# Kernel tuning notes

Measured on AMD Instinct MI355X. Metric: run time of the kernel, lower is better.

Reference implementation:

```python
import jax, jax.numpy as jnp
import numpy as np

B, H, N, C = 4, 16, 1024, 64
D = H * C  # d_model = 1024


def setup_inputs() -> dict:
    key = jax.random.key(0)
    ks = jax.random.split(key, 6)
    q = jax.random.normal(ks[0], (B, H, N, C), dtype=jnp.float32)
    k = jax.random.normal(ks[1], (B, H, N, C), dtype=jnp.float32)
    v = jax.random.normal(ks[2], (B, H, N, C), dtype=jnp.float32)
    pe = jax.random.normal(ks[3], (1, H, N, N), dtype=jnp.float32)
    # Mlp(h*c): fc1 D->D, SiLU, fc2 D->D (stored as [in, out] for x @ W)
    w1 = jax.random.normal(ks[4], (D, D), dtype=jnp.float32) * (D ** -0.5)
    b1 = jnp.zeros((D,), dtype=jnp.float32)
    w2 = jax.random.normal(ks[5], (D, D), dtype=jnp.float32) * (D ** -0.5)
    b2 = jnp.zeros((D,), dtype=jnp.float32)
    return {"q": q, "k": k, "v": v, "pe": pe,
            "w1": w1, "b1": b1, "w2": w2, "b2": b2}


def reference(q, k, v, pe, w1, b1, w2, b2):
    b, h, n, c = q.shape
    scale = c ** (-0.5)
    # scores: [b,h,n,n]; softmax FIRST, then add pe bias (post-softmax bias)
    scores = jnp.einsum('bhnc,bhmc->bhnm', q, k) * scale
    attn = pe + jax.nn.softmax(scores, axis=-1)
    ctx = jnp.einsum('bhnm,bhmc->bhnc', attn, v)
    # [b,h,n,c] -> [b,n,h*c]
    out = ctx.transpose(0, 2, 1, 3).reshape(b, n, h * c)
    # Mlp: fc1 -> SiLU -> fc2 (dropout is identity at eval)
    hdn = jax.nn.silu(out @ w1 + b1)
    return hdn @ w2 + b2
```

## Files before the change

### kernel.cpp

```cpp
#include <hip/hip_runtime.h>

#define B_ 4
#define H_ 16
#define N_ 1024
#define C_ 64
#define D_ 1024

typedef _Float16 half8 __attribute__((ext_vector_type(8)));
typedef _Float16 half4v __attribute__((ext_vector_type(4)));
typedef float f32x4 __attribute__((ext_vector_type(4)));
typedef float f32x16 __attribute__((ext_vector_type(16)));
typedef unsigned int uint4v __attribute__((ext_vector_type(4)));

#define MFMA16(a, b, c) __builtin_amdgcn_mfma_f32_16x16x32_f16(a, b, c, 0, 0, 0)
#define MFMA32(a, b, c) __builtin_amdgcn_mfma_f32_32x32x16_f16(a, b, c, 0, 0, 0)
#define SM_SHIFT 6.0f

static __device__ __forceinline__ unsigned pk2(float a, float b) {
  auto h = __builtin_amdgcn_cvt_pkrtz(a, b);
  return __builtin_bit_cast(unsigned, h);
}
static __device__ __forceinline__ void swap32(unsigned& a, unsigned& b) {
  asm volatile("v_permlane32_swap_b32 %0, %1" : "+v"(a), "+v"(b));
}
static __device__ __forceinline__ void gload16(const void* g, void* l) {
  __builtin_amdgcn_global_load_lds(
      (const __attribute__((address_space(1))) unsigned int*)g,
      (__attribute__((address_space(3))) unsigned int*)l, 16, 0, 0);
}

__global__ __launch_bounds__(256) void transpose_cvt(
    const float* __restrict__ in, _Float16* __restrict__ outp,
    int in_stride, int out_stride, long in_bstride, long out_bstride)
{
  __shared__ float t[64][65];
  const int tid = threadIdx.x;
  const int r0 = blockIdx.x * 64, c0 = blockIdx.y * 64;
  const float* inb = in + (size_t)blockIdx.z * in_bstride;
  _Float16* outb = outp + (size_t)blockIdx.z * out_bstride;
#pragma unroll
  for (int i = 0; i < 4; ++i) {
    int idx = i * 256 + tid;
    int r = idx >> 4, c4 = (idx & 15) << 2;
    float4 a = *(const float4*)(inb + (size_t)(r0 + r) * in_stride + c0 + c4);
    t[r][c4] = a.x; t[r][c4 + 1] = a.y; t[r][c4 + 2] = a.z; t[r][c4 + 3] = a.w;
  }
  __syncthreads();
#pragma unroll
  for (int i = 0; i < 2; ++i) {
    int idx = i * 256 + tid;
    int rr = idx >> 3, c8 = (idx & 7) << 3;
    half8 hv;
#pragma unroll
    for (int j = 0; j < 8; ++j) hv[j] = (_Float16)t[c8 + j][rr];
    *(half8*)(outb + (size_t)(c0 + rr) * out_stride + r0 + c8) = hv;
  }
}

__global__ __launch_bounds__(256, 1) void pev_kernel(
    const float* __restrict__ pe, const _Float16* __restrict__ vth,
    _Float16* __restrict__ xpe)
{
  __shared__ __align__(16) _Float16 a_lds[2][64][72];
  __shared__ __align__(16) _Float16 b_lds[2][256][72];
  const int tid = threadIdx.x;
  const int n0 = blockIdx.x * 64;
  const int h = blockIdx.y;
  const float* peb = pe + (size_t)h * N_ * N_ + (size_t)n0 * N_;

  const int lane = tid & 63, w = tid >> 6;
  const int l15 = lane & 15, quad = lane >> 4;
  const int wrow = (w >> 1) * 32, wcol = (w & 1) * 128;

  const int ar[4] = { tid >> 4, (256 + tid) >> 4, (512 + tid) >> 4, (768 + tid) >> 4 };
  const int ac4 = (tid & 15) << 2;
  const _Float16* bsrc[8];
  int brow[8], bk8[8];
#pragma unroll
  for (int i = 0; i < 8; ++i) {
    int idx = i * 256 + tid;
    int col = idx >> 3, k8 = (idx & 7) << 3;
    int b = col >> 6, c = col & 63;
    bsrc[i] = vth + ((size_t)(b * H_ + h) * C_ + c) * N_ + k8;
    brow[i] = col;
    bk8[i] = k8;
  }

  f32x4 acc[2][8];
#pragma unroll
  for (int rt = 0; rt < 2; ++rt)
#pragma unroll
    for (int ct = 0; ct < 8; ++ct) acc[rt][ct] = (f32x4){0.f, 0.f, 0.f, 0.f};

  float4 areg[4];
  half8 breg[8];
#pragma unroll
  for (int i = 0; i < 4; ++i) areg[i] = *(const float4*)(peb + (size_t)ar[i] * N_ + ac4);
#pragma unroll
  for (int i = 0; i < 8; ++i) breg[i] = *(const half8*)(bsrc[i]);
#pragma unroll
  for (int i = 0; i < 4; ++i) {
    half4v hv = {(_Float16)areg[i].x, (_Float16)areg[i].y,
                 (_Float16)areg[i].z, (_Float16)areg[i].w};
    *(half4v*)&a_lds[0][ar[i]][ac4] = hv;
  }
#pragma unroll
  for (int i = 0; i < 8; ++i) *(half8*)&b_lds[0][brow[i]][bk8[i]] = breg[i];
#pragma unroll
  for (int i = 0; i < 4; ++i)
    areg[i] = *(const float4*)(peb + (size_t)ar[i] * N_ + 64 + ac4);
#pragma unroll
  for (int i = 0; i < 8; ++i) breg[i] = *(const half8*)(bsrc[i] + 64);
  __syncthreads();

  for (int kt = 0; kt < 16; ++kt) {
    const int cur = kt & 1;
    if (kt < 15) {
#pragma unroll
      for (int i = 0; i < 4; ++i) {
        half4v hv = {(_Float16)areg[i].x, (_Float16)areg[i].y,
                     (_Float16)areg[i].z, (_Float16)areg[i].w};
        *(half4v*)&a_lds[cur ^ 1][ar[i]][ac4] = hv;
      }
#pragma unroll
      for (int i = 0; i < 8; ++i) *(half8*)&b_lds[cur ^ 1][brow[i]][bk8[i]] = breg[i];
    }
    if (kt < 14) {
      int m0 = (kt + 2) * 64;
#pragma unroll
      for (int i = 0; i < 4; ++i)
        areg[i] = *(const float4*)(peb + (size_t)ar[i] * N_ + m0 + ac4);
#pragma unroll
      for (int i = 0; i < 8; ++i) breg[i] = *(const half8*)(bsrc[i] + m0);
    }
#pragma unroll
    for (int s = 0; s < 2; ++s) {
      half8 af[2], bf[8];
#pragma unroll
      for (int rt = 0; rt < 2; ++rt)
        af[rt] = *(const half8*)&a_lds[cur][wrow + rt * 16 + l15][s * 32 + quad * 8];
#pragma unroll
      for (int ct = 0; ct < 8; ++ct)
        bf[ct] = *(const half8*)&b_lds[cur][wcol + ct * 16 + l15][s * 32 + quad * 8];
#pragma unroll
      for (int rt = 0; rt < 2; ++rt)
#pragma unroll
        for (int ct = 0; ct < 8; ++ct)
          acc[rt][ct] = MFMA16(af[rt], bf[ct], acc[rt][ct]);
    }
    __syncthreads();
  }

#pragma unroll
  for (int rt = 0; rt < 2; ++rt)
#pragma unroll
    for (int ct = 0; ct < 8; ++ct) {
      int col = wcol + ct * 16 + l15;
      int b = col >> 6, c = col & 63;
#pragma unroll
      for (int r = 0; r < 4; ++r) {
        int nrow = n0 + wrow + rt * 16 + quad * 4 + r;
        xpe[(size_t)(b * N_ + nrow) * D_ + h * C_ + c] = (_Float16)acc[rt][ct][r];
      }
    }
}

__global__ __launch_bounds__(256, 2) void attn_kernel(
    const float* __restrict__ q, const float* __restrict__ k,
    const _Float16* __restrict__ vth, const _Float16* __restrict__ xpe,
    _Float16* __restrict__ Xh)
{
  __shared__ __align__(16) _Float16 ks[2][2][64][72];
  __shared__ __align__(16) _Float16 vst[2][2][64][72];
  __shared__ float lbuf[128];

  const int tid = threadIdx.x;
  const int bh = blockIdx.x & 63;
  const int qt = blockIdx.x >> 6;
  const int h = bh & (H_ - 1);
  const int b = bh >> 4;
  const int q0 = qt * 128;

  const float* kb = k + (size_t)bh * N_ * C_;
  const _Float16* vb = vth + (size_t)bh * C_ * N_;

  const int lane = tid & 63;
  const int w = tid >> 6;
  const int l31 = lane & 31;
  const int hh = lane >> 5;

  const int sr = tid >> 4, sc4 = (tid & 15) << 2;
  const int vr = tid >> 3, vc8 = (tid & 7) << 3;

  half8 qf[4];
  const float* qrow = q + ((size_t)bh * N_ + q0 + 32 * w + l31) * C_;
#pragma unroll
  for (int sc = 0; sc < 4; ++sc) {
    const float* qp = qrow + 16 * sc + 8 * hh;
    float4 t0 = *(const float4*)qp;
    float4 t1 = *(const float4*)(qp + 4);
    half8 hv = { (_Float16)(t0.x * 0.125f), (_Float16)(t0.y * 0.125f),
                 (_Float16)(t0.z * 0.125f), (_Float16)(t0.w * 0.125f),
                 (_Float16)(t1.x * 0.125f), (_Float16)(t1.y * 0.125f),
                 (_Float16)(t1.z * 0.125f), (_Float16)(t1.w * 0.125f) };
    qf[sc] = hv;
  }

  f32x16 Os2[2];
  Os2[0] = (f32x16)(0.f); Os2[1] = (f32x16)(0.f);
  float l4[4] = {0.f, 0.f, 0.f, 0.f};

  float4 kreg[8];
  uint4 vreg[4];

#pragma unroll
  for (int s = 0; s < 2; ++s) {
#pragma unroll
    for (int i = 0; i < 4; ++i)
      kreg[s * 4 + i] = *(const float4*)(kb + (size_t)(s * 64 + sr + i * 16) * C_ + sc4);
#pragma unroll
    for (int i = 0; i < 2; ++i)
      vreg[s * 2 + i] = *(const uint4*)(vb + (size_t)(vr + i * 32) * N_ + s * 64 + vc8);
  }
#pragma unroll
  for (int s = 0; s < 2; ++s) {
#pragma unroll
    for (int i = 0; i < 4; ++i) {
      float4 kv = kreg[s * 4 + i];
      half4v hk = {(_Float16)kv.x, (_Float16)kv.y, (_Float16)kv.z, (_Float16)kv.w};
      *(half4v*)&ks[0][s][sr + i * 16][sc4] = hk;
    }
#pragma unroll
    for (int i = 0; i < 2; ++i) *(uint4*)&vst[0][s][vr + i * 32][vc8] = vreg[s * 2 + i];
  }
#pragma unroll
  for (int s = 0; s < 2; ++s) {
#pragma unroll
    for (int i = 0; i < 4; ++i)
      kreg[s * 4 + i] = *(const float4*)(kb + (size_t)(128 + s * 64 + sr + i * 16) * C_ + sc4);
#pragma unroll
    for (int i = 0; i < 2; ++i)
      vreg[s * 2 + i] = *(const uint4*)(vb + (size_t)(vr + i * 32) * N_ + 128 + s * 64 + vc8);
  }
  __syncthreads();

  for (int p = 0; p < 8; ++p) {
    const int cur = p & 1;
    if (p < 7) {
#pragma unroll
      for (int s = 0; s < 2; ++s) {
#pragma unroll
        for (int i = 0; i < 4; ++i) {
          float4 kv = kreg[s * 4 + i];
          half4v hk = {(_Float16)kv.x, (_Float16)kv.y, (_Float16)kv.z, (_Float16)kv.w};
          *(half4v*)&ks[cur ^ 1][s][sr + i * 16][sc4] = hk;
        }
#pragma unroll
        for (int i = 0; i < 2; ++i)
          *(uint4*)&vst[cur ^ 1][s][vr + i * 32][vc8] = vreg[s * 2 + i];
      }
    }
    if (p < 6) {
      int m0 = (p + 2) * 128;
#pragma unroll
      for (int s = 0; s < 2; ++s) {
#pragma unroll
        for (int i = 0; i < 4; ++i)
          kreg[s * 4 + i] = *(const float4*)(kb + (size_t)(m0 + s * 64 + sr + i * 16) * C_ + sc4);
#pragma unroll
        for (int i = 0; i < 2; ++i)
          vreg[s * 2 + i] = *(const uint4*)(vb + (size_t)(vr + i * 32) * N_ + m0 + s * 64 + vc8);
      }
    }

    half8 pa[2][4];
#pragma unroll
    for (int s = 0; s < 2; ++s) {
      f32x16 sacc2[2];
      sacc2[0] = (f32x16)(0.f); sacc2[1] = (f32x16)(0.f);
#pragma unroll
      for (int sc = 0; sc < 4; ++sc) {
        half8 ak0 = *(const half8*)&ks[cur][s][l31][16 * sc + 8 * hh];
        half8 ak1 = *(const half8*)&ks[cur][s][32 + l31][16 * sc + 8 * hh];
        sacc2[0] = MFMA32(ak0, qf[sc], sacc2[0]);
        sacc2[1] = MFMA32(ak1, qf[sc], sacc2[1]);
      }
#pragma unroll
      for (int kbt = 0; kbt < 2; ++kbt) {
        float pv[16];
#pragma unroll
        for (int r = 0; r < 16; ++r) {
          pv[r] = __expf(sacc2[kbt][r] - SM_SHIFT);
          l4[r & 3] += pv[r];
        }
#pragma unroll
        for (int sp = 0; sp < 2; ++sp) {
          const int rb = 8 * sp;
          unsigned wa = pk2(pv[rb + 0], pv[rb + 1]);
          unsigned wb = pk2(pv[rb + 4], pv[rb + 5]);
          unsigned wc = pk2(pv[rb + 2], pv[rb + 3]);
          unsigned wd = pk2(pv[rb + 6], pv[rb + 7]);
          swap32(wa, wb);
          swap32(wc, wd);
          uint4v pw = {wa, wc, wb, wd};
          pa[s][kbt * 2 + sp] = __builtin_bit_cast(half8, pw);
        }
      }
    }

#pragma unroll
    for (int s = 0; s < 2; ++s)
#pragma unroll
      for (int st = 0; st < 4; ++st) {
        half8 bv0 = *(const half8*)&vst[cur][s][l31][16 * st + 8 * hh];
        half8 bv1 = *(const half8*)&vst[cur][s][32 + l31][16 * st + 8 * hh];
        Os2[0] = MFMA32(pa[s][st], bv0, Os2[0]);
        Os2[1] = MFMA32(pa[s][st], bv1, Os2[1]);
      }

    __syncthreads();
  }

  float l = (l4[0] + l4[1]) + (l4[2] + l4[3]);
  l += __shfl_xor(l, 32);
  lbuf[32 * w + l31] = 1.0f / l;

#pragma unroll
  for (int reg = 0; reg < 16; ++reg) {
    const int qi = (reg & 3) + 8 * (reg >> 2) + 4 * hh;
    const float li = lbuf[32 * w + qi];
    const size_t row = (size_t)(b * N_ + q0 + 32 * w + qi);
#pragma unroll
    for (int ct = 0; ct < 2; ++ct) {
      size_t o = row * D_ + h * C_ + 32 * ct + l31;
      Xh[o] = (_Float16)(Os2[ct][reg] * li + (float)xpe[o]);
    }
  }
}

template <bool SILU, typename OT>
__global__ __launch_bounds__(256, 2) void mlp_kernel(
    const _Float16* __restrict__ X, const _Float16* __restrict__ Wt,
    const float* __restrict__ bias, OT* __restrict__ Y)
{
  __shared__ __align__(16) _Float16 a_lds[2][128 * 64];
  __shared__ __align__(16) _Float16 b_lds[2][64 * 64];
  const int tid = threadIdx.x;
  const int id = blockIdx.x;
  const int xcd = id & 7, j = id >> 3;
  const int m0 = (xcd * 4 + (j & 3)) * 128;
  const int n0 = (j >> 2) * 64;
  const int lane = tid & 63, w = tid >> 6;
  const int wr = (w >> 1) * 64, wc = (w & 1) * 32;
  const int l15 = lane & 15, quad = lane >> 4;

  const int lrow8 = lane >> 3;
  const int lg = lane & 7;

  f32x4 acc[4][2];
#pragma unroll
  for (int rt = 0; rt < 4; ++rt)
#pragma unroll
    for (int ct = 0; ct < 2; ++ct) acc[rt][ct] = (f32x4){0.f, 0.f, 0.f, 0.f};

#define STAGE_MLP(buf, k0)                                                     \
  {                                                                            \
    _Float16* abase = &a_lds[buf][(w * 4) * 8 * 64];                           \
    _Float16* bbase = &b_lds[buf][(w * 2) * 8 * 64];                           \
    _Float16* ab = abase;                                                      \
    _Float16* bb = bbase;                                                      \
    _Float16* dummy = ab; (void)dummy;                                         \
    int ar0 = w * 32;                                                          \
    int br0 = w * 16;                                                          \
    for (int jj = 0; jj < 4; ++jj) {                                           \
      int r = ar0 + jj * 8 + lrow8;                                            \
      const _Float16* src = X + (size_t)(m0 + r) * D_ + (k0) + ((lg ^ (r & 7)) << 3); \
      gload16(src, &a_lds[buf][(ar0 + jj * 8) * 64]);                          \
    }                                                                          \
    for (int jj = 0; jj < 2; ++jj) {                                           \
      int r = br0 + jj * 8 + lrow8;                                            \
      const _Float16* src = Wt + (size_t)(n0 + r) * D_ + (k0) + ((lg ^ (r & 7)) << 3); \
      gload16(src, &b_lds[buf][(br0 + jj * 8) * 64]);                          \
    }                                                                          \
  }

  STAGE_MLP(0, 0);
  __syncthreads();

  for (int kt = 0; kt < 16; ++kt) {
    const int cur = kt & 1;
    if (kt < 15) STAGE_MLP(cur ^ 1, (kt + 1) * 64);
#pragma unroll
    for (int s = 0; s < 2; ++s) {
      half8 af[4], bf[2];
#pragma unroll
      for (int rt = 0; rt < 4; ++rt) {
        int row = wr + rt * 16 + l15;
        af[rt] = *(const half8*)&a_lds[cur][row * 64 + (((s * 4 + quad) ^ (row & 7)) << 3)];
      }
#pragma unroll
      for (int ct = 0; ct < 2; ++ct) {
        int row = wc + ct * 16 + l15;
        bf[ct] = *(const half8*)&b_lds[cur][row * 64 + (((s * 4 + quad) ^ (row & 7)) << 3)];
      }
#pragma unroll
      for (int rt = 0; rt < 4; ++rt)
#pragma unroll
        for (int ct = 0; ct < 2; ++ct)
          acc[rt][ct] = MFMA16(af[rt], bf[ct], acc[rt][ct]);
    }
    __syncthreads();
  }
#undef STAGE_MLP

  float bv[2];
#pragma unroll
  for (int ct = 0; ct < 2; ++ct) bv[ct] = bias[n0 + wc + ct * 16 + l15];
#pragma unroll
  for (int rt = 0; rt < 4; ++rt)
#pragma unroll
    for (int ct = 0; ct < 2; ++ct)
#pragma unroll
      for (int r = 0; r < 4; ++r) {
        float val = acc[rt][ct][r] + bv[ct];
        if (SILU) val = val / (1.f + __expf(-val));
        int row = m0 + wr + rt * 16 + quad * 4 + r;
        int col = n0 + wc + ct * 16 + l15;
        Y[(size_t)row * D_ + col] = (OT)val;
      }
}

extern "C" void kernel_launch(void* const* d_in, const int* in_sizes, int n_in,
                              void* d_out, int out_size, void* d_ws, size_t ws_size,
                              hipStream_t stream) {
  const float* q  = (const float*)d_in[0];
  const float* k  = (const float*)d_in[1];
  const float* v  = (const float*)d_in[2];
  const float* pe = (const float*)d_in[3];
  const float* w1 = (const float*)d_in[4];
  const float* b1 = (const float*)d_in[5];
  const float* w2 = (const float*)d_in[6];
  const float* b2 = (const float*)d_in[7];
  float* out = (float*)d_out;

  _Float16* Xh  = (_Float16*)d_out;
  _Float16* vth = (_Float16*)((char*)d_out + (size_t)8 * 1024 * 1024);
  _Float16* xpeH1 = (_Float16*)d_ws;
  _Float16* w1t = (_Float16*)((char*)d_ws + (size_t)8 * 1024 * 1024);
  _Float16* w2t = (_Float16*)((char*)d_ws + (size_t)10 * 1024 * 1024);

  transpose_cvt<<<dim3(16, 16, 1), 256, 0, stream>>>(w1, w1t, D_, D_, 0, 0);
  transpose_cvt<<<dim3(16, 16, 1), 256, 0, stream>>>(w2, w2t, D_, D_, 0, 0);
  transpose_cvt<<<dim3(16, 1, B_ * H_), 256, 0, stream>>>(
      v, vth, C_, N_, (long)N_ * C_, (long)N_ * C_);
  pev_kernel<<<dim3(N_ / 64, H_), 256, 0, stream>>>(pe, vth, xpeH1);
  attn_kernel<<<dim3(B_ * H_ * (N_ / 128)), 256, 0, stream>>>(q, k, vth, xpeH1, Xh);
  mlp_kernel<true, _Float16><<<dim3(512), 256, 0, stream>>>(Xh, w1t, b1, xpeH1);
  mlp_kernel<false, float><<<dim3(512), 256, 0, stream>>>(xpeH1, w2t, b2, out);
}
```

Baseline: 245.2 us.

## Widen pe@V kernel to 512 threads and load V fragments directly from global in attention

The pe@V kernel now runs 8 waves per block instead of 4, halving per-thread staging loads and accumulator tiles so more waves are available to hide the fp32 pe stream. In the attention kernel, the V tile is no longer staged through LDS; each lane loads its MFMA B-fragments straight from the transposed fp16 V in global memory at the start of each iteration. This cuts LDS traffic and shared memory use, which may allow higher occupancy. The trade-off is that the V loads are no longer prefetched two iterations ahead, so their global latency sits right before the MFMAs, and loads are duplicated across waves. Dead pointer code in the MLP staging macro is also removed.

Measured after the change: 253.9 us. 1.04x slower.

```diff
diff --git a/kernel.cpp b/kernel.cpp
--- a/kernel.cpp
+++ b/kernel.cpp
@@ -57,7 +57,7 @@
   }
 }
 
-__global__ __launch_bounds__(256, 1) void pev_kernel(
+__global__ __launch_bounds__(512, 1) void pev_kernel(
     const float* __restrict__ pe, const _Float16* __restrict__ vth,
     _Float16* __restrict__ xpe)
 {
@@ -70,15 +70,15 @@
 
   const int lane = tid & 63, w = tid >> 6;
   const int l15 = lane & 15, quad = lane >> 4;
-  const int wrow = (w >> 1) * 32, wcol = (w & 1) * 128;
-
-  const int ar[4] = { tid >> 4, (256 + tid) >> 4, (512 + tid) >> 4, (768 + tid) >> 4 };
+  const int wrow = (w >> 2) * 32, wcol = (w & 3) * 64;
+
+  const int ar[2] = { tid >> 4, (512 + tid) >> 4 };
   const int ac4 = (tid & 15) << 2;
-  const _Float16* bsrc[8];
-  int brow[8], bk8[8];
-#pragma unroll
-  for (int i = 0; i < 8; ++i) {
-    int idx = i * 256 + tid;
+  const _Float16* bsrc[4];
+  int brow[4], bk8[4];
+#pragma unroll
+  for (int i = 0; i < 4; ++i) {
+    int idx = i * 512 + tid;
     int col = idx >> 3, k8 = (idx & 7) << 3;
     int b = col >> 6, c = col & 63;
     bsrc[i] = vth + ((size_t)(b * H_ + h) * C_ + c) * N_ + k8;
@@ -86,66 +86,66 @@
     bk8[i] = k8;
   }
 
-  f32x4 acc[2][8];
+  f32x4 acc[2][4];
 #pragma unroll
   for (int rt = 0; rt < 2; ++rt)
 #pragma unroll
-    for (int ct = 0; ct < 8; ++ct) acc[rt][ct] = (f32x4){0.f, 0.f, 0.f, 0.f};
-
-  float4 areg[4];
-  half8 breg[8];
-#pragma unroll
-  for (int i = 0; i < 4; ++i) areg[i] = *(const float4*)(peb + (size_t)ar[i] * N_ + ac4);
-#pragma unroll
-  for (int i = 0; i < 8; ++i) breg[i] = *(const half8*)(bsrc[i]);
-#pragma unroll
-  for (int i = 0; i < 4; ++i) {
+    for (int ct = 0; ct < 4; ++ct) acc[rt][ct] = (f32x4){0.f, 0.f, 0.f, 0.f};
+
+  float4 areg[2];
+  half8 breg[4];
+#pragma unroll
+  for (int i = 0; i < 2; ++i) areg[i] = *(const float4*)(peb + (size_t)ar[i] * N_ + ac4);
+#pragma unroll
+  for (int i = 0; i < 4; ++i) breg[i] = *(const half8*)(bsrc[i]);
+#pragma unroll
+  for (int i = 0; i < 2; ++i) {
     half4v hv = {(_Float16)areg[i].x, (_Float16)areg[i].y,
                  (_Float16)areg[i].z, (_Float16)areg[i].w};
     *(half4v*)&a_lds[0][ar[i]][ac4] = hv;
   }
 #pragma unroll
-  for (int i = 0; i < 8; ++i) *(half8*)&b_lds[0][brow[i]][bk8[i]] = breg[i];
-#pragma unroll
-  for (int i = 0; i < 4; ++i)
+  for (int i = 0; i < 4; ++i) *(half8*)&b_lds[0][brow[i]][bk8[i]] = breg[i];
+#pragma unroll
+  for (int i = 0; i < 2; ++i)
     areg[i] = *(const float4*)(peb + (size_t)ar[i] * N_ + 64 + ac4);
 #pragma unroll
-  for (int i = 0; i < 8; ++i) breg[i] = *(const half8*)(bsrc[i] + 64);
+  for (int i = 0; i < 4; ++i) breg[i] = *(const half8*)(bsrc[i] + 64);
   __syncthreads();
 
   for (int kt = 0; kt < 16; ++kt) {
     const int cur = kt & 1;
     if (kt < 15) {
 #pragma unroll
-      for (int i = 0; i < 4; ++i) {
+      for (int i = 0; i < 2; ++i) {
         half4v hv = {(_Float16)areg[i].x, (_Float16)areg[i].y,
                      (_Float16)areg[i].z, (_Float16)areg[i].w};
         *(half4v*)&a_lds[cur ^ 1][ar[i]][ac4] = hv;
       }
 #pragma unroll
-      for (int i = 0; i < 8; ++i) *(half8*)&b_lds[cur ^ 1][brow[i]][bk8[i]] = breg[i];
+      for (int i = 0; i < 4; ++i) *(half8*)&b_lds[cur ^ 1][brow[i]][bk8[i]] = breg[i];
     }
     if (kt < 14) {
       int m0 = (kt + 2) * 64;
 #pragma unroll
-      for (int i = 0; i < 4; ++i)
+      for (int i = 0; i < 2; ++i)
         areg[i] = *(const float4*)(peb + (size_t)ar[i] * N_ + m0 + ac4);
 #pragma unroll
-      for (int i = 0; i < 8; ++i) breg[i] = *(const half8*)(bsrc[i] + m0);
+      for (int i = 0; i < 4; ++i) breg[i] = *(const half8*)(bsrc[i] + m0);
     }
 #pragma unroll
     for (int s = 0; s < 2; ++s) {
-      half8 af[2], bf[8];
+      half8 af[2], bf[4];
 #pragma unroll
       for (int rt = 0; rt < 2; ++rt)
         af[rt] = *(const half8*)&a_lds[cur][wrow + rt * 16 + l15][s * 32 + quad * 8];
 #pragma unroll
-      for (int ct = 0; ct < 8; ++ct)
+      for (int ct = 0; ct < 4; ++ct)
         bf[ct] = *(const half8*)&b_lds[cur][wcol + ct * 16 + l15][s * 32 + quad * 8];
 #pragma unroll
       for (int rt = 0; rt < 2; ++rt)
 #pragma unroll
-        for (int ct = 0; ct < 8; ++ct)
+        for (int ct = 0; ct < 4; ++ct)
           acc[rt][ct] = MFMA16(af[rt], bf[ct], acc[rt][ct]);
     }
     __syncthreads();
@@ -154,7 +154,7 @@
 #pragma unroll
   for (int rt = 0; rt < 2; ++rt)
 #pragma unroll
-    for (int ct = 0; ct < 8; ++ct) {
+    for (int ct = 0; ct < 4; ++ct) {
       int col = wcol + ct * 16 + l15;
       int b = col >> 6, c = col & 63;
 #pragma unroll
@@ -171,7 +171,6 @@
     _Float16* __restrict__ Xh)
 {
   __shared__ __align__(16) _Float16 ks[2][2][64][72];
-  __shared__ __align__(16) _Float16 vst[2][2][64][72];
   __shared__ float lbuf[128];
 
   const int tid = threadIdx.x;
@@ -190,7 +189,9 @@
   const int hh = lane >> 5;
 
   const int sr = tid >> 4, sc4 = (tid & 15) << 2;
-  const int vr = tid >> 3, vc8 = (tid & 7) << 3;
+
+  const _Float16* vr0 = vb + (size_t)l31 * N_ + 8 * hh;
+  const _Float16* vr1 = vb + (size_t)(32 + l31) * N_ + 8 * hh;
 
   half8 qf[4];
   const float* qrow = q + ((size_t)bh * N_ + q0 + 32 * w + l31) * C_;
@@ -211,19 +212,14 @@
   float l4[4] = {0.f, 0.f, 0.f, 0.f};
 
   float4 kreg[8];
-  uint4 vreg[4];
-
-#pragma unroll
-  for (int s = 0; s < 2; ++s) {
+
+#pragma unroll
+  for (int s = 0; s < 2; ++s)
 #pragma unroll
     for (int i = 0; i < 4; ++i)
       kreg[s * 4 + i] = *(const float4*)(kb + (size_t)(s * 64 + sr + i * 16) * C_ + sc4);
 #pragma unroll
-    for (int i = 0; i < 2; ++i)
-      vreg[s * 2 + i] = *(const uint4*)(vb + (size_t)(vr + i * 32) * N_ + s * 64 + vc8);
-  }
-#pragma unroll
-  for (int s = 0; s < 2; ++s) {
+  for (int s = 0; s < 2; ++s)
 #pragma unroll
     for (int i = 0; i < 4; ++i) {
       float4 kv = kreg[s * 4 + i];
@@ -231,46 +227,42 @@
       *(half4v*)&ks[0][s][sr + i * 16][sc4] = hk;
     }
 #pragma unroll
-    for (int i = 0; i < 2; ++i) *(uint4*)&vst[0][s][vr + i * 32][vc8] = vreg[s * 2 + i];
-  }
-#pragma unroll
-  for (int s = 0; s < 2; ++s) {
+  for (int s = 0; s < 2; ++s)
 #pragma unroll
     for (int i = 0; i < 4; ++i)
       kreg[s * 4 + i] = *(const float4*)(kb + (size_t)(128 + s * 64 + sr + i * 16) * C_ + sc4);
-#pragma unroll
-    for (int i = 0; i < 2; ++i)
-      vreg[s * 2 + i] = *(const uint4*)(vb + (size_t)(vr + i * 32) * N_ + 128 + s * 64 + vc8);
-  }
   __syncthreads();
 
   for (int p = 0; p < 8; ++p) {
     const int cur = p & 1;
+
+    uint4 vfr[2][4][2];
+#pragma unroll
+    for (int s = 0; s < 2; ++s)
+#pragma unroll
+      for (int st = 0; st < 4; ++st) {
+        const int off = p * 128 + s * 64 + st * 16;
+        vfr[s][st][0] = *(const uint4*)(vr0 + off);
+        vfr[s][st][1] = *(const uint4*)(vr1 + off);
+      }
+
     if (p < 7) {
 #pragma unroll
-      for (int s = 0; s < 2; ++s) {
+      for (int s = 0; s < 2; ++s)
 #pragma unroll
         for (int i = 0; i < 4; ++i) {
           float4 kv = kreg[s * 4 + i];
           half4v hk = {(_Float16)kv.x, (_Float16)kv.y, (_Float16)kv.z, (_Float16)kv.w};
           *(half4v*)&ks[cur ^ 1][s][sr + i * 16][sc4] = hk;
         }
-#pragma unroll
-        for (int i = 0; i < 2; ++i)
-          *(uint4*)&vst[cur ^ 1][s][vr + i * 32][vc8] = vreg[s * 2 + i];
-      }
     }
     if (p < 6) {
       int m0 = (p + 2) * 128;
 #pragma unroll
-      for (int s = 0; s < 2; ++s) {
+      for (int s = 0; s < 2; ++s)
 #pragma unroll
         for (int i = 0; i < 4; ++i)
           kreg[s * 4 + i] = *(const float4*)(kb + (size_t)(m0 + s * 64 + sr + i * 16) * C_ + sc4);
-#pragma unroll
-        for (int i = 0; i < 2; ++i)
-          vreg[s * 2 + i] = *(const uint4*)(vb + (size_t)(vr + i * 32) * N_ + m0 + s * 64 + vc8);
-      }
     }
 
     half8 pa[2][4];
@@ -312,10 +304,8 @@
     for (int s = 0; s < 2; ++s)
 #pragma unroll
       for (int st = 0; st < 4; ++st) {
-        half8 bv0 = *(const half8*)&vst[cur][s][l31][16 * st + 8 * hh];
-        half8 bv1 = *(const half8*)&vst[cur][s][32 + l31][16 * st + 8 * hh];
-        Os2[0] = MFMA32(pa[s][st], bv0, Os2[0]);
-        Os2[1] = MFMA32(pa[s][st], bv1, Os2[1]);
+        Os2[0] = MFMA32(pa[s][st], __builtin_bit_cast(half8, vfr[s][st][0]), Os2[0]);
+        Os2[1] = MFMA32(pa[s][st], __builtin_bit_cast(half8, vfr[s][st][1]), Os2[1]);
       }
 
     __syncthreads();
@@ -365,11 +355,6 @@
 
 #define STAGE_MLP(buf, k0)                                                     \
   {                                                                            \
-    _Float16* abase = &a_lds[buf][(w * 4) * 8 * 64];                           \
-    _Float16* bbase = &b_lds[buf][(w * 2) * 8 * 64];                           \
-    _Float16* ab = abase;                                                      \
-    _Float16* bb = bbase;                                                      \
-    _Float16* dummy = ab; (void)dummy;                                         \
     int ar0 = w * 32;                                                          \
     int br0 = w * 16;                                                          \
     for (int jj = 0; jj < 4; ++jj) {                                           \
@@ -453,7 +438,7 @@
   transpose_cvt<<<dim3(16, 16, 1), 256, 0, stream>>>(w2, w2t, D_, D_, 0, 0);
   transpose_cvt<<<dim3(16, 1, B_ * H_), 256, 0, stream>>>(
       v, vth, C_, N_, (long)N_ * C_, (long)N_ * C_);
-  pev_kernel<<<dim3(N_ / 64, H_), 256, 0, stream>>>(pe, vth, xpeH1);
+  pev_kernel<<<dim3(N_ / 64, H_), 512, 0, stream>>>(pe, vth, xpeH1);
   attn_kernel<<<dim3(B_ * H_ * (N_ / 128)), 256, 0, stream>>>(q, k, vth, xpeH1, Xh);
   mlp_kernel<true, _Float16><<<dim3(512), 256, 0, stream>>>(Xh, w1t, b1, xpeH1);
   mlp_kernel<false, float><<<dim3(512), 256, 0, stream>>>(xpeH1, w2t, b2, out);
```
